# Kernel tuning notes

Measured on AMD Instinct MI355X. Metric: run time of the kernel, lower is better.

Reference implementation:

```python
import jax, jax.numpy as jnp
import numpy as np

B, S, V = 512, 256, 10      # batch, s_node_num, v_node_num
E, H = 128, 128             # embedding, lstm hidden
D = 2 * H                   # num_directions * hidden
PENALTY = 1.0e6
STD = 0.1


def _cell(x, h, c, Wih, Whh, b):
    # PyTorch LSTM cell, gate order i, f, g, o; b = b_ih + b_hh
    g = x @ Wih.T + h @ Whh.T + b
    i, f, gg, o = jnp.split(g, 4, axis=-1)
    c = jax.nn.sigmoid(f) * c + jax.nn.sigmoid(i) * jnp.tanh(gg)
    h = jax.nn.sigmoid(o) * jnp.tanh(c)
    return h, c


def setup_inputs() -> dict:
    key = jax.random.key(0)
    ks = jax.random.split(key, 25)
    w = lambda k, shp: (jax.random.normal(k, shp, jnp.float32) * STD)
    return {
        's_node_indexes': jax.random.randint(ks[0], (B, S), 0, S, dtype=jnp.int32),
        's_inputs': jax.random.uniform(ks[1], (B, S, 3), jnp.float32),
        'v_input': jax.random.uniform(ks[2], (V, 3), jnp.float32) * 0.5,
        'W_embed': w(ks[3], (E, 1)),
        'enc_Wih_f': w(ks[4], (4 * H, E)), 'enc_Whh_f': w(ks[5], (4 * H, H)), 'enc_b_f': w(ks[6], (4 * H,)),
        'enc_Wih_b': w(ks[7], (4 * H, E)), 'enc_Whh_b': w(ks[8], (4 * H, H)), 'enc_b_b': w(ks[9], (4 * H,)),
        'dec_Wih_f': w(ks[10], (4 * H, D)), 'dec_Whh_f': w(ks[11], (4 * H, H)), 'dec_b_f': w(ks[12], (4 * H,)),
        'dec_Wih_b': w(ks[13], (4 * H, D)), 'dec_Whh_b': w(ks[14], (4 * H, H)), 'dec_b_b': w(ks[15], (4 * H,)),
        'W_ref': w(ks[16], (D, D)), 'W_q': w(ks[17], (D, D)), 'v_w': w(ks[18], (D,)),
        'W_ref2': w(ks[19], (D, D)), 'W_q2': w(ks[20], (D, D)), 'v2_w': w(ks[21], (D,)),
    }


def reference(s_node_indexes, s_inputs, v_input, W_embed,
              enc_Wih_f, enc_Whh_f, enc_b_f, enc_Wih_b, enc_Whh_b, enc_b_b,
              dec_Wih_f, dec_Whh_f, dec_b_f, dec_Wih_b, dec_Whh_b, dec_b_b,
              W_ref, W_q, v_w, W_ref2, W_q2, v2_w):
    Bn, Sn = s_node_indexes.shape
    # Embed: snode resource -> Linear(1, E, bias=False)
    emb = s_inputs[:, :, 0:1] @ W_embed.T            # (B, S, E)
    xs = jnp.swapaxes(emb, 0, 1)                     # (S, B, E)
    h0 = jnp.zeros((Bn, H), jnp.float32)
    c0 = jnp.zeros((Bn, H), jnp.float32)

    def enc_scan(Wih, Whh, b, seq):
        def step(carry, x):
            h, c = carry
            h, c = _cell(x, h, c, Wih, Whh, b)
            return (h, c), h
        (hT, cT), hs = jax.lax.scan(step, (h0, c0), seq)
        return hs, hT, cT

    hs_f, hf, cf = enc_scan(enc_Wih_f, enc_Whh_f, enc_b_f, xs)
    hs_b, hb, cb = enc_scan(enc_Wih_b, enc_Whh_b, enc_b_b, xs[::-1])
    Enc = jnp.swapaxes(jnp.concatenate([hs_f, hs_b[::-1]], axis=-1), 0, 1)  # (B, S, D)
    h_state = jnp.stack([hf, hb])                    # (2, B, H)
    c_state = jnp.stack([cf, cb])

    refE = Enc @ W_ref.T                             # (B, S, D) precomputed (dropout p=0)
    ref2E = Enc @ W_ref2.T

    def dec_step(carry, vcpu):
        dec_in, h, c, played = carry                 # dec_in (B, D)
        hf_, cf_ = _cell(dec_in, h[0], c[0], dec_Wih_f, dec_Whh_f, dec_b_f)
        hb_, cb_ = _cell(dec_in, h[1], c[1], dec_Wih_b, dec_Whh_b, dec_b_b)
        dec_out = jnp.concatenate([hf_, hb_], axis=-1)                       # (B, D)
        cannot = (s_inputs[:, :, 0] < vcpu).astype(jnp.float32) + played     # (B, S)
        ow = jnp.tanh(refE + (dec_out @ W_q.T)[:, None, :]) @ v_w - PENALTY * cannot
        att = jax.nn.softmax(jnp.tanh(ref2E + (dec_in @ W_q2.T)[:, None, :]) @ v2_w, axis=1)
        new_in = jnp.einsum('bs,bsd->bd', att, Enc)
        sel = jnp.argmax(ow, axis=1)
        played = played + jax.nn.one_hot(sel, Sn, dtype=jnp.float32)
        return (new_in, jnp.stack([hf_, hb_]), jnp.stack([cf_, cb_]), played), (ow, sel)

    init = (jnp.zeros((Bn, D), jnp.float32), h_state, c_state, jnp.zeros((Bn, Sn), jnp.float32))
    _, (output_weights, sels) = jax.lax.scan(dec_step, init, v_input[:, 0])
    shuffled = sels.T                                # (B, V)
    original = jnp.take_along_axis(s_node_indexes, shuffled, axis=1)
    return original, shuffled, output_weights        # output_weights: (V, B, S)
```

## Files before the change

kernel.cpp:

```cpp
#include <hip/hip_runtime.h>
#include <math.h>

#define cB 512
#define cS 256
#define cV 10
#define cE 128
#define cH 128
#define cD 256
#define cG 512
#define PEN 1.0e6f
#define S1 224
#define PADK 40

typedef _Float16 half8_t __attribute__((ext_vector_type(8)));
typedef _Float16 half4_t __attribute__((ext_vector_type(4)));
typedef float f32x4 __attribute__((ext_vector_type(4)));

#define DOT4(acc, wv, hv)                                   \
    do {                                                    \
        acc = fmaf((wv).x, (hv).x, acc);                    \
        acc = fmaf((wv).y, (hv).y, acc);                    \
        acc = fmaf((wv).z, (hv).z, acc);                    \
        acc = fmaf((wv).w, (hv).w, acc);                    \
    } while (0)

__device__ __forceinline__ float sigmf(float x) { return 1.0f / (1.0f + expf(-x)); }

__global__ __launch_bounds__(512, 1) void k_encoder(
    const float* __restrict__ s_inputs, const float* __restrict__ W_embed,
    const float* __restrict__ Wih_f, const float* __restrict__ Whh_f, const float* __restrict__ b_f,
    const float* __restrict__ Wih_b, const float* __restrict__ Whh_b, const float* __restrict__ b_b,
    _Float16* __restrict__ Ehi, _Float16* __restrict__ Elo,
    float* __restrict__ h_state, float* __restrict__ c_state)
{
    const int dir = blockIdx.x >> 8;
    const int b0  = (blockIdx.x & 255) * 2;
    const float* __restrict__ Wih = dir ? Wih_b : Wih_f;
    const float* __restrict__ Whh = dir ? Whh_b : Whh_f;
    const float* __restrict__ bv  = dir ? b_b   : b_f;
    const int j = threadIdx.x;

    __shared__ __align__(16) float a_in[2][cS];
    __shared__ __align__(16) float hbuf[2][cH];
    __shared__ __align__(16) float gbuf[2][cG];

    {
        int bb = j >> 8, s = j & 255;
        a_in[bb][s] = s_inputs[((size_t)(b0 + bb) * cS + s) * 3];
    }

    float4 w[32];
#pragma unroll
    for (int kk = 0; kk < 32; ++kk) {
        w[kk] = *(const float4*)&Whh[(size_t)j * cH + kk * 4];
        asm volatile("" : "+v"(w[kk].x), "+v"(w[kk].y), "+v"(w[kk].z), "+v"(w[kk].w));
    }

    float u = 0.0f;
#pragma unroll 8
    for (int e = 0; e < cE; ++e) u = fmaf(Wih[(size_t)j * cE + e], W_embed[e], u);
    const float bj = bv[j];

    const int uk = j & 127, ub = (j >> 7) & 1;
    float c_reg = 0.0f;
    float h_last = 0.0f;
    if (j < 256) hbuf[ub][uk] = 0.0f;
    __syncthreads();

    for (int p = 0; p < cS; ++p) {
        const int s = dir ? (cS - 1 - p) : p;
        float acc0 = fmaf(a_in[0][s], u, bj);
        float acc1 = fmaf(a_in[1][s], u, bj);
#pragma unroll
        for (int kk = 0; kk < 32; ++kk) {
            const float4 wv = w[kk];
            const float4 h0 = *(const float4*)&hbuf[0][kk * 4];
            const float4 h1 = *(const float4*)&hbuf[1][kk * 4];
            DOT4(acc0, wv, h0);
            DOT4(acc1, wv, h1);
        }
        gbuf[0][j] = acc0;
        gbuf[1][j] = acc1;
        __syncthreads();

        if (j < 256) {
            float gi = gbuf[ub][uk];
            float gf = gbuf[ub][128 + uk];
            float gg = gbuf[ub][256 + uk];
            float go = gbuf[ub][384 + uk];
            float i_ = sigmf(gi), f_ = sigmf(gf), g_ = tanhf(gg), o_ = sigmf(go);
            c_reg = fmaf(f_, c_reg, i_ * g_);
            float hn = o_ * tanhf(c_reg);
            h_last = hn;
            hbuf[ub][uk] = hn;
            const size_t eidx = ((size_t)(b0 + ub) * cS + s) * cD + dir * cH + uk;
            _Float16 hh = (_Float16)hn;
            Ehi[eidx] = hh;
            Elo[eidx] = (_Float16)(hn - (float)hh);
        }
        __syncthreads();
    }
    if (j < 256) {
        h_state[((size_t)dir * cB + b0 + ub) * cH + uk] = h_last;
        c_state[((size_t)dir * cB + b0 + ub) * cH + uk] = c_reg;
    }
}

__global__ void k_split_w(const float* __restrict__ W1, const float* __restrict__ W2,
                          _Float16* __restrict__ Whi1, _Float16* __restrict__ Wlo1,
                          _Float16* __restrict__ Whi2, _Float16* __restrict__ Wlo2)
{
    const int i = blockIdx.x * 256 + threadIdx.x;
    {
        float a = W1[i]; _Float16 h = (_Float16)a;
        Whi1[i] = h; Wlo1[i] = (_Float16)(a - (float)h);
    }
    {
        float a = W2[i]; _Float16 h = (_Float16)a;
        Whi2[i] = h; Wlo2[i] = (_Float16)(a - (float)h);
    }
}

__global__ __launch_bounds__(256) void k_head_mat(
    const _Float16* __restrict__ Ahi, const _Float16* __restrict__ Alo,
    const _Float16* __restrict__ Whi, const _Float16* __restrict__ Wlo,
    float* __restrict__ outv)
{
    const int tid = threadIdx.x;
    const int w = tid >> 6, l = tid & 63;
    const int m0 = blockIdx.x * 64;

    __shared__ __align__(16) _Float16 As[2][64][PADK];
    __shared__ __align__(16) _Float16 Ws[2][256][PADK];

    const int r = tid >> 2, kq = tid & 3;
    size_t arow;
    {
        const int m = m0 + r;
        const int s = m >> 9, b = m & 511;
        arow = ((size_t)b * cS + s) * cD;
    }
    const size_t wrow = (size_t)tid * cD;

    f32x4 acc[16];
#pragma unroll
    for (int i = 0; i < 16; ++i) acc[i] = (f32x4){0.f, 0.f, 0.f, 0.f};

    const int fr = w * 16 + (l & 15);
    const int kc = (l >> 4) * 8;

    for (int k0 = 0; k0 < 256; k0 += 32) {
        __syncthreads();
        *(uint4*)&As[0][r][kq * 8] = *(const uint4*)&Ahi[arow + k0 + kq * 8];
        *(uint4*)&As[1][r][kq * 8] = *(const uint4*)&Alo[arow + k0 + kq * 8];
#pragma unroll
        for (int q4 = 0; q4 < 4; ++q4) {
            *(uint4*)&Ws[0][tid][q4 * 8] = *(const uint4*)&Whi[wrow + k0 + q4 * 8];
            *(uint4*)&Ws[1][tid][q4 * 8] = *(const uint4*)&Wlo[wrow + k0 + q4 * 8];
        }
        __syncthreads();

        const half8_t ahi = *(const half8_t*)&As[0][fr][kc];
        const half8_t alo = *(const half8_t*)&As[1][fr][kc];
#pragma unroll
        for (int nf = 0; nf < 16; ++nf) {
            const int n = nf * 16 + (l & 15);
            const half8_t bhi = *(const half8_t*)&Ws[0][n][kc];
            const half8_t blo = *(const half8_t*)&Ws[1][n][kc];
            acc[nf] = __builtin_amdgcn_mfma_f32_16x16x32_f16(ahi, bhi, acc[nf], 0, 0, 0);
            acc[nf] = __builtin_amdgcn_mfma_f32_16x16x32_f16(ahi, blo, acc[nf], 0, 0, 0);
            acc[nf] = __builtin_amdgcn_mfma_f32_16x16x32_f16(alo, bhi, acc[nf], 0, 0, 0);
        }
    }
#pragma unroll
    for (int nf = 0; nf < 16; ++nf)
#pragma unroll
        for (int rr = 0; rr < 4; ++rr) {
            const int m = w * 16 + ((l >> 4) << 2) + rr;
            outv[(size_t)(m0 + m) * cD + nf * 16 + (l & 15)] = acc[nf][rr];
        }
}

template <int MODE>
__global__ __launch_bounds__(512, 2) void k_head2(
    const _Float16* __restrict__ Ahi, const _Float16* __restrict__ Alo,
    const _Float16* __restrict__ Whi, const _Float16* __restrict__ Wlo,
    const float* __restrict__ qv, const float* __restrict__ vv,
    float* __restrict__ outv)
{
    const int tid = threadIdx.x;
    const int l = tid & 63;
    const int w = tid >> 6;
    const int wm = w >> 2, wn = w & 3;
    const int g = l >> 4, li = l & 15;
    const int m0 = blockIdx.x * 128;

    __shared__ __align__(16) _Float16 Ah[128][PADK];
    __shared__ __align__(16) _Float16 Al[128][PADK];
    __shared__ __align__(16) _Float16 Wh[256][PADK];
    __shared__ __align__(16) _Float16 Wl[256][PADK];
    __shared__ __align__(16) float qs[4][cD];
    __shared__ __align__(16) float vs[cD];
    __shared__ float spart[4][128];

    if (MODE == 0) {
        const int b = m0 >> 8;
        if (tid < 256) qs[0][tid] = qv[(size_t)b * cD + tid];
        else           vs[tid - 256] = vv[tid - 256];
    } else {
        const int b0 = m0 >> 5;
        qs[tid >> 8][tid & 255] = qv[(size_t)(b0 + (tid >> 8)) * cD + (tid & 255)];
        const int i2 = tid + 512;
        qs[i2 >> 8][i2 & 255] = qv[(size_t)(b0 + (i2 >> 8)) * cD + (i2 & 255)];
        if (tid < 256) vs[tid] = vv[tid];
    }

    const int ar = tid >> 2, aq = tid & 3;
    size_t arow;
    {
        const int m = m0 + ar;
        if (MODE == 0) arow = (size_t)m * cD;
        else { const int b = m >> 5, s = S1 + (m & 31); arow = ((size_t)b * cS + s) * cD; }
    }

    f32x4 acc[4][4];
#pragma unroll
    for (int mi = 0; mi < 4; ++mi)
#pragma unroll
        for (int ni = 0; ni < 4; ++ni) acc[mi][ni] = (f32x4){0.f, 0.f, 0.f, 0.f};

    for (int k0 = 0; k0 < 256; k0 += 32) {
        __syncthreads();
        *(uint4*)&Ah[ar][aq * 8] = *(const uint4*)&Ahi[arow + k0 + aq * 8];
        *(uint4*)&Al[ar][aq * 8] = *(const uint4*)&Alo[arow + k0 + aq * 8];
        *(uint4*)&Wh[ar][aq * 8] = *(const uint4*)&Whi[(size_t)ar * cD + k0 + aq * 8];
        *(uint4*)&Wl[ar][aq * 8] = *(const uint4*)&Wlo[(size_t)ar * cD + k0 + aq * 8];
        *(uint4*)&Wh[ar + 128][aq * 8] = *(const uint4*)&Whi[(size_t)(ar + 128) * cD + k0 + aq * 8];
        *(uint4*)&Wl[ar + 128][aq * 8] = *(const uint4*)&Wlo[(size_t)(ar + 128) * cD + k0 + aq * 8];
        __syncthreads();

        half8_t ah[4], al[4];
#pragma unroll
        for (int mi = 0; mi < 4; ++mi) {
            ah[mi] = *(const half8_t*)&Ah[wm * 64 + mi * 16 + li][g * 8];
            al[mi] = *(const half8_t*)&Al[wm * 64 + mi * 16 + li][g * 8];
        }
#pragma unroll
        for (int ni = 0; ni < 4; ++ni) {
            const half8_t bh = *(const half8_t*)&Wh[wn * 64 + ni * 16 + li][g * 8];
            const half8_t bl = *(const half8_t*)&Wl[wn * 64 + ni * 16 + li][g * 8];
#pragma unroll
            for (int mi = 0; mi < 4; ++mi) {
                acc[mi][ni] = __builtin_amdgcn_mfma_f32_16x16x32_f16(ah[mi], bh, acc[mi][ni], 0, 0, 0);
                acc[mi][ni] = __builtin_amdgcn_mfma_f32_16x16x32_f16(ah[mi], bl, acc[mi][ni], 0, 0, 0);
                acc[mi][ni] = __builtin_amdgcn_mfma_f32_16x16x32_f16(al[mi], bh, acc[mi][ni], 0, 0, 0);
            }
        }
    }

    float val = 0.f;
#pragma unroll
    for (int mi = 0; mi < 4; ++mi)
#pragma unroll
        for (int rr = 0; rr < 4; ++rr) {
            const int row = wm * 64 + mi * 16 + g * 4 + rr;
            const int bl = (MODE == 1) ? (row >> 5) : 0;
            float p = 0.f;
#pragma unroll
            for (int ni = 0; ni < 4; ++ni) {
                const int c = wn * 64 + ni * 16 + li;
                p = fmaf(vs[c], tanhf(acc[mi][ni][rr] + qs[bl][c]), p);
            }
            p += __shfl_xor(p, 1);
            p += __shfl_xor(p, 2);
            p += __shfl_xor(p, 4);
            p += __shfl_xor(p, 8);
            if (li == mi * 4 + rr) val = p;
        }
    {
        const int row_out = wm * 64 + (li >> 2) * 16 + g * 4 + (li & 3);
        spart[wn][row_out] = val;
    }
    __syncthreads();
    if (tid < 128)
        outv[m0 + tid] = spart[0][tid] + spart[1][tid] + spart[2][tid] + spart[3][tid];
}

__global__ __launch_bounds__(256, 4) void k_fold(
    const float* __restrict__ refC, const float* __restrict__ q1v,
    const float* __restrict__ v_w, float* __restrict__ sc1lo)
{
    const int tid = threadIdx.x;
    const int m0 = blockIdx.x * 64;
    const int r = tid >> 2, p = tid & 3;
    const int m = m0 + r;
    const int b = m & 511;
    __shared__ float red[64][4];

    const float* row  = refC + (size_t)m * cD + p * 64;
    const float* qrow = q1v + (size_t)b * cD + p * 64;
    const float* vrow = v_w + p * 64;
    float s = 0.f;
#pragma unroll 4
    for (int d = 0; d < 64; d += 4) {
        const float4 rv4 = *(const float4*)&row[d];
        const float4 q4  = *(const float4*)&qrow[d];
        const float4 v4  = *(const float4*)&vrow[d];
        s = fmaf(v4.x, tanhf(rv4.x + q4.x), s);
        s = fmaf(v4.y, tanhf(rv4.y + q4.y), s);
        s = fmaf(v4.z, tanhf(rv4.z + q4.z), s);
        s = fmaf(v4.w, tanhf(rv4.w + q4.w), s);
    }
    red[r][p] = s;
    __syncthreads();
    if (tid < 64)
        sc1lo[m0 + tid] = red[tid][0] + red[tid][1] + red[tid][2] + red[tid][3];
}

__global__ __launch_bounds__(512, 2) void k_dec_cells(
    const float* __restrict__ dec_in,
    const float* __restrict__ Wih_f, const float* __restrict__ Whh_f, const float* __restrict__ b_f,
    const float* __restrict__ Wih_b, const float* __restrict__ Whh_b, const float* __restrict__ b_b,
    float* __restrict__ h_state, float* __restrict__ c_state, float* __restrict__ dec_out)
{
    const int cell = blockIdx.x >> 7;
    const int b0 = (blockIdx.x & 127) * 4;
    const float* __restrict__ Wih = cell ? Wih_b : Wih_f;
    const float* __restrict__ Whh = cell ? Whh_b : Whh_f;
    const float* __restrict__ bv  = cell ? b_b   : b_f;
    const int j = threadIdx.x;

    __shared__ __align__(16) float xin[4][cD];
    __shared__ __align__(16) float hin[4][cH];
    __shared__ __align__(16) float gbuf[4][cG];

    for (int idx = j; idx < 4 * cD; idx += 512) {
        int bb = idx >> 8, k = idx & 255;
        xin[bb][k] = dec_in[(size_t)(b0 + bb) * cD + k];
    }
    {
        int bb = j >> 7, k = j & 127;
        hin[bb][k] = h_state[((size_t)cell * cB + b0 + bb) * cH + k];
    }
    __syncthreads();

    float a0 = bv[j];
    float a1 = a0, a2 = a0, a3 = a0;
#pragma unroll 4
    for (int kk = 0; kk < 64; ++kk) {
        const float4 wv = *(const float4*)&Wih[(size_t)j * cD + kk * 4];
        const float4 x0 = *(const float4*)&xin[0][kk * 4]; DOT4(a0, wv, x0);
        const float4 x1 = *(const float4*)&xin[1][kk * 4]; DOT4(a1, wv, x1);
        const float4 x2 = *(const float4*)&xin[2][kk * 4]; DOT4(a2, wv, x2);
        const float4 x3 = *(const float4*)&xin[3][kk * 4]; DOT4(a3, wv, x3);
    }
#pragma unroll 4
    for (int kk = 0; kk < 32; ++kk) {
        const float4 wv = *(const float4*)&Whh[(size_t)j * cH + kk * 4];
        const float4 h0 = *(const float4*)&hin[0][kk * 4]; DOT4(a0, wv, h0);
        const float4 h1 = *(const float4*)&hin[1][kk * 4]; DOT4(a1, wv, h1);
        const float4 h2 = *(const float4*)&hin[2][kk * 4]; DOT4(a2, wv, h2);
        const float4 h3 = *(const float4*)&hin[3][kk * 4]; DOT4(a3, wv, h3);
    }
    gbuf[0][j] = a0; gbuf[1][j] = a1; gbuf[2][j] = a2; gbuf[3][j] = a3;
    __syncthreads();

    const int uk = j & 127, ub = j >> 7;
    const float gi = gbuf[ub][uk];
    const float gf = gbuf[ub][128 + uk];
    const float gg = gbuf[ub][256 + uk];
    const float go = gbuf[ub][384 + uk];
    const size_t sidx = ((size_t)cell * cB + b0 + ub) * cH + uk;
    const float c_old = c_state[sidx];
    const float i_ = sigmf(gi), f_ = sigmf(gf), g_ = tanhf(gg), o_ = sigmf(go);
    const float cn = fmaf(f_, c_old, i_ * g_);
    const float hn = o_ * tanhf(cn);
    c_state[sidx] = cn;
    h_state[sidx] = hn;
    dec_out[(size_t)(b0 + ub) * cD + cell * cH + uk] = hn;
}

__global__ __launch_bounds__(256, 2) void k_qproj(
    const float* __restrict__ dec_out, const float* __restrict__ dec_in_old,
    const float* __restrict__ W_q, const float* __restrict__ W_q2,
    float* __restrict__ q1v, float* __restrict__ q2v)
{
    const int b = blockIdx.x;
    const int tid = threadIdx.x;
    __shared__ __align__(16) float dout[cD];
    __shared__ __align__(16) float din[cD];
    dout[tid] = dec_out[(size_t)b * cD + tid];
    din[tid]  = dec_in_old[(size_t)b * cD + tid];
    __syncthreads();
    float s1 = 0.0f, s2 = 0.0f;
#pragma unroll 4
    for (int kk = 0; kk < 64; ++kk) {
        const float4 w1 = *(const float4*)&W_q[(size_t)tid * cD + kk * 4];
        const float4 w2 = *(const float4*)&W_q2[(size_t)tid * cD + kk * 4];
        const float4 x1 = *(const float4*)&dout[kk * 4];
        const float4 x2 = *(const float4*)&din[kk * 4];
        DOT4(s1, w1, x1);
        DOT4(s2, w2, x2);
    }
    q1v[(size_t)b * cD + tid] = s1;
    q2v[(size_t)b * cD + tid] = s2;
}

__global__ __launch_bounds__(256, 2) void k_finish(
    const float* __restrict__ sc1lo, const float* __restrict__ sc1hi,
    const float* __restrict__ sc2,
    const _Float16* __restrict__ Ehi, const _Float16* __restrict__ Elo,
    const float* __restrict__ s_inputs, const int* __restrict__ s_node_indexes,
    const float* __restrict__ v_input, float* __restrict__ played,
    float* __restrict__ dec_in_new, float* __restrict__ outp, int t)
{
    const int b = blockIdx.x;
    const int tid = threadIdx.x;
    const int lane = tid & 63;
    const int wv = tid >> 6;

    __shared__ __align__(16) float atr[cS];
    __shared__ __align__(16) float part[4][cD];
    __shared__ float rv[cS];
    __shared__ int   ri[cS];

    const float owv = (tid < S1) ? sc1lo[(size_t)tid * cB + b]
                                 : sc1hi[(size_t)b * (cS - S1) + (tid - S1)];
    atr[tid] = sc2[(size_t)b * cS + tid];

    const float vcpu = v_input[t * 3];
    float val;
    {
        const float a0 = s_inputs[((size_t)b * cS + tid) * 3];
        const float can = (a0 < vcpu ? 1.0f : 0.0f) + played[(size_t)b * cS + tid];
        val = owv - PEN * can;
        outp[2 * cB * cV + ((size_t)t * cB + b) * cS + tid] = val;
    }
    rv[tid] = val; ri[tid] = tid;
    __syncthreads();
#pragma unroll
    for (int off = 128; off > 0; off >>= 1) {
        if (tid < off) {
            const float v2 = rv[tid + off]; const int i2 = ri[tid + off];
            const float v1 = rv[tid];       const int i1 = ri[tid];
            if (v2 > v1 || (v2 == v1 && i2 < i1)) { rv[tid] = v2; ri[tid] = i2; }
        }
        __syncthreads();
    }
    const int sel = ri[0];
    __syncthreads();
    if (tid == 0) {
        played[(size_t)b * cS + sel] += 1.0f;
        outp[(size_t)b * cV + t] = (float)s_node_indexes[(size_t)b * cS + sel];
        outp[(size_t)cB * cV + (size_t)b * cV + t] = (float)sel;
    }

    rv[tid] = atr[tid];
    __syncthreads();
#pragma unroll
    for (int off = 128; off > 0; off >>= 1) {
        if (tid < off) { const float v2 = rv[tid + off]; if (v2 > rv[tid]) rv[tid] = v2; }
        __syncthreads();
    }
    const float mx = rv[0];
    __syncthreads();
    const float ex = expf(atr[tid] - mx);
    rv[tid] = ex;
    __syncthreads();
#pragma unroll
    for (int off = 128; off > 0; off >>= 1) {
        if (tid < off) rv[tid] += rv[tid + off];
        __syncthreads();
    }
    const float ssum = rv[0];
    __syncthreads();
    atr[tid] = ex / ssum;
    __syncthreads();

    {
        float4 acc = make_float4(0.f, 0.f, 0.f, 0.f);
        for (int s2i = wv * 64; s2i < wv * 64 + 64; ++s2i) {
            const float a = atr[s2i];
            const size_t eidx = ((size_t)b * cS + s2i) * cD + lane * 4;
            const half4_t h4 = *(const half4_t*)&Ehi[eidx];
            const half4_t l4 = *(const half4_t*)&Elo[eidx];
            acc.x = fmaf(a, (float)h4[0] + (float)l4[0], acc.x);
            acc.y = fmaf(a, (float)h4[1] + (float)l4[1], acc.y);
            acc.z = fmaf(a, (float)h4[2] + (float)l4[2], acc.z);
            acc.w = fmaf(a, (float)h4[3] + (float)l4[3], acc.w);
        }
        *(float4*)&part[wv][lane * 4] = acc;
    }
    __syncthreads();
    dec_in_new[(size_t)b * cD + tid] =
        part[0][tid] + part[1][tid] + part[2][tid] + part[3][tid];
}

extern "C" void kernel_launch(void* const* d_in, const int* in_sizes, int n_in,
                              void* d_out, int out_size, void* d_ws, size_t ws_size,
                              hipStream_t stream)
{
    (void)in_sizes; (void)n_in; (void)out_size; (void)ws_size;

    const int*   s_node = (const int*)  d_in[0];
    const float* s_inp  = (const float*)d_in[1];
    const float* v_inp  = (const float*)d_in[2];
    const float* W_emb  = (const float*)d_in[3];
    const float* eWih_f = (const float*)d_in[4];
    const float* eWhh_f = (const float*)d_in[5];
    const float* eb_f   = (const float*)d_in[6];
    const float* eWih_b = (const float*)d_in[7];
    const float* eWhh_b = (const float*)d_in[8];
    const float* eb_b   = (const float*)d_in[9];
    const float* dWih_f = (const float*)d_in[10];
    const float* dWhh_f = (const float*)d_in[11];
    const float* db_f   = (const float*)d_in[12];
    const float* dWih_b = (const float*)d_in[13];
    const float* dWhh_b = (const float*)d_in[14];
    const float* db_b   = (const float*)d_in[15];
    const float* W_ref  = (const float*)d_in[16];
    const float* W_q    = (const float*)d_in[17];
    const float* v_w    = (const float*)d_in[18];
    const float* W_ref2 = (const float*)d_in[19];
    const float* W_q2   = (const float*)d_in[20];
    const float* v2_w   = (const float*)d_in[21];

    float* out = (float*)d_out;
    const size_t ENCSZ = (size_t)cB * cS * cD;
    const size_t SMALL = (size_t)cB * cD;

    char* p = (char*)d_ws;
    _Float16* Ehi = (_Float16*)p; p += ENCSZ * 2;
    _Float16* Elo = (_Float16*)p; p += ENCSZ * 2;
    float* refC  = (float*)p;     p += (size_t)S1 * cB * cD * 4;
    _Float16* Whi1 = (_Float16*)p; p += (size_t)cD * cD * 2;
    _Float16* Wlo1 = (_Float16*)p; p += (size_t)cD * cD * 2;
    _Float16* Whi2 = (_Float16*)p; p += (size_t)cD * cD * 2;
    _Float16* Wlo2 = (_Float16*)p; p += (size_t)cD * cD * 2;
    float* hst    = (float*)p; p += SMALL * 4;
    float* cst    = (float*)p; p += SMALL * 4;
    float* din0   = (float*)p; p += SMALL * 4;
    float* din1   = (float*)p; p += SMALL * 4;
    float* doutb  = (float*)p; p += SMALL * 4;
    float* played = (float*)p; p += SMALL * 4;
    float* q1v    = (float*)p; p += SMALL * 4;
    float* q2v    = (float*)p; p += SMALL * 4;
    float* sc2    = (float*)p; p += SMALL * 4;
    float* sc1lo  = (float*)p; p += (size_t)S1 * cB * 4;
    float* sc1hi  = (float*)p; p += (size_t)(cS - S1) * cB * 4;

    hipMemsetAsync(played, 0, SMALL * sizeof(float), stream);
    hipMemsetAsync(din0,   0, SMALL * sizeof(float), stream);

    k_split_w<<<256, 256, 0, stream>>>(W_ref, W_ref2, Whi1, Wlo1, Whi2, Wlo2);

    k_encoder<<<512, 512, 0, stream>>>(s_inp, W_emb, eWih_f, eWhh_f, eb_f,
                                       eWih_b, eWhh_b, eb_b, Ehi, Elo, hst, cst);

    k_head_mat<<<(S1 * cB) / 64, 256, 0, stream>>>(Ehi, Elo, Whi1, Wlo1, refC);

    for (int t = 0; t < cV; ++t) {
        float* di_old = (t & 1) ? din1 : din0;
        float* di_new = (t & 1) ? din0 : din1;
        k_dec_cells<<<256, 512, 0, stream>>>(di_old, dWih_f, dWhh_f, db_f,
                                             dWih_b, dWhh_b, db_b, hst, cst, doutb);
        k_qproj<<<512, 256, 0, stream>>>(doutb, di_old, W_q, W_q2, q1v, q2v);
        k_head2<0><<<(cB * cS) / 128, 512, 0, stream>>>(Ehi, Elo, Whi2, Wlo2,
                                                        q2v, v2_w, sc2);
        k_head2<1><<<(cB * (cS - S1)) / 128, 512, 0, stream>>>(Ehi, Elo, Whi1, Wlo1,
                                                               q1v, v_w, sc1hi);
        k_fold<<<(S1 * cB) / 64, 256, 0, stream>>>(refC, q1v, v_w, sc1lo);

        k_finish<<<512, 256, 0, stream>>>(sc1lo, sc1hi, sc2, Ehi, Elo,
                                          s_inp, s_node, v_inp, played, di_new, out, t);
    }
}
```

Measured before the change: 3.656 ms.

## Restructure encoder LSTM: 4 batch rows per block, split-K across thread halves

The encoder kernel now processes four batch rows per block with 1024 threads. Each half of the threads handles 64 of the 128 hidden-state columns, and the two partial gate sums are combined through shared memory. The input-projection vector u is precomputed once by a small new kernel instead of being recomputed in every block. The aim is to halve the block count and the weight registers per thread while reusing each weight load across more batch rows. The cost is an extra shared-memory reduction each step and 1024-thread barriers on the sequential 256-step recurrence.

```diff
diff --git a/kernel.cpp b/kernel.cpp
--- a/kernel.cpp
+++ b/kernel.cpp
@@ -26,83 +26,96 @@
 
 __device__ __forceinline__ float sigmf(float x) { return 1.0f / (1.0f + expf(-x)); }
 
-__global__ __launch_bounds__(512, 1) void k_encoder(
-    const float* __restrict__ s_inputs, const float* __restrict__ W_embed,
-    const float* __restrict__ Wih_f, const float* __restrict__ Whh_f, const float* __restrict__ b_f,
-    const float* __restrict__ Wih_b, const float* __restrict__ Whh_b, const float* __restrict__ b_b,
+__global__ void k_uprep(const float* __restrict__ Wih_f, const float* __restrict__ Wih_b,
+                        const float* __restrict__ W_embed, float* __restrict__ uvec)
+{
+    const int j = threadIdx.x;
+    const float* __restrict__ Wih = blockIdx.x ? Wih_b : Wih_f;
+    float u = 0.f;
+#pragma unroll 8
+    for (int e = 0; e < cE; ++e) u = fmaf(Wih[(size_t)j * cE + e], W_embed[e], u);
+    uvec[blockIdx.x * cG + j] = u;
+}
+
+__global__ __launch_bounds__(1024, 4) void k_encoder(
+    const float* __restrict__ s_inputs, const float* __restrict__ uvec,
+    const float* __restrict__ Whh_f, const float* __restrict__ b_f,
+    const float* __restrict__ Whh_b, const float* __restrict__ b_b,
     _Float16* __restrict__ Ehi, _Float16* __restrict__ Elo,
     float* __restrict__ h_state, float* __restrict__ c_state)
 {
-    const int dir = blockIdx.x >> 8;
-    const int b0  = (blockIdx.x & 255) * 2;
-    const float* __restrict__ Wih = dir ? Wih_b : Wih_f;
+    const int dir = blockIdx.x >> 7;
+    const int b0  = (blockIdx.x & 127) * 4;
     const float* __restrict__ Whh = dir ? Whh_b : Whh_f;
     const float* __restrict__ bv  = dir ? b_b   : b_f;
-    const int j = threadIdx.x;
-
-    __shared__ __align__(16) float a_in[2][cS];
-    __shared__ __align__(16) float hbuf[2][cH];
-    __shared__ __align__(16) float gbuf[2][cG];
-
-    {
-        int bb = j >> 8, s = j & 255;
-        a_in[bb][s] = s_inputs[((size_t)(b0 + bb) * cS + s) * 3];
-    }
-
-    float4 w[32];
-#pragma unroll
-    for (int kk = 0; kk < 32; ++kk) {
-        w[kk] = *(const float4*)&Whh[(size_t)j * cH + kk * 4];
-        asm volatile("" : "+v"(w[kk].x), "+v"(w[kk].y), "+v"(w[kk].z), "+v"(w[kk].w));
-    }
-
-    float u = 0.0f;
-#pragma unroll 8
-    for (int e = 0; e < cE; ++e) u = fmaf(Wih[(size_t)j * cE + e], W_embed[e], u);
-    const float bj = bv[j];
-
-    const int uk = j & 127, ub = (j >> 7) & 1;
-    float c_reg = 0.0f;
-    float h_last = 0.0f;
-    if (j < 256) hbuf[ub][uk] = 0.0f;
+    const int tid = threadIdx.x;
+    const int j = tid & 511;
+    const int hf = tid >> 9;
+
+    __shared__ __align__(16) float a_in[4][cS];
+    __shared__ __align__(16) float hbuf[4][cH];
+    __shared__ __align__(16) float gpart[4][2][516];
+
+    a_in[tid >> 8][tid & 255] =
+        s_inputs[((size_t)(b0 + (tid >> 8)) * cS + (tid & 255)) * 3];
+
+    float4 w[16];
+#pragma unroll
+    for (int kk = 0; kk < 16; ++kk)
+        w[kk] = *(const float4*)&Whh[(size_t)j * cH + hf * 64 + kk * 4];
+
+    const float uj = (hf == 0) ? uvec[dir * cG + j] : 0.f;
+    const float bj = (hf == 0) ? bv[j] : 0.f;
+
+    const int ur = tid >> 7, uk = tid & 127;
+    float c_reg = 0.f, h_last = 0.f;
+    if (tid < 512) hbuf[ur][uk] = 0.f;
     __syncthreads();
 
     for (int p = 0; p < cS; ++p) {
         const int s = dir ? (cS - 1 - p) : p;
-        float acc0 = fmaf(a_in[0][s], u, bj);
-        float acc1 = fmaf(a_in[1][s], u, bj);
-#pragma unroll
-        for (int kk = 0; kk < 32; ++kk) {
+        float acc0 = fmaf(a_in[0][s], uj, bj);
+        float acc1 = fmaf(a_in[1][s], uj, bj);
+        float acc2 = fmaf(a_in[2][s], uj, bj);
+        float acc3 = fmaf(a_in[3][s], uj, bj);
+#pragma unroll
+        for (int kk = 0; kk < 16; ++kk) {
             const float4 wv = w[kk];
-            const float4 h0 = *(const float4*)&hbuf[0][kk * 4];
-            const float4 h1 = *(const float4*)&hbuf[1][kk * 4];
+            const float4 h0 = *(const float4*)&hbuf[0][hf * 64 + kk * 4];
             DOT4(acc0, wv, h0);
+            const float4 h1 = *(const float4*)&hbuf[1][hf * 64 + kk * 4];
             DOT4(acc1, wv, h1);
-        }
-        gbuf[0][j] = acc0;
-        gbuf[1][j] = acc1;
-        __syncthreads();
-
-        if (j < 256) {
-            float gi = gbuf[ub][uk];
-            float gf = gbuf[ub][128 + uk];
-            float gg = gbuf[ub][256 + uk];
-            float go = gbuf[ub][384 + uk];
-            float i_ = sigmf(gi), f_ = sigmf(gf), g_ = tanhf(gg), o_ = sigmf(go);
+            const float4 h2 = *(const float4*)&hbuf[2][hf * 64 + kk * 4];
+            DOT4(acc2, wv, h2);
+            const float4 h3 = *(const float4*)&hbuf[3][hf * 64 + kk * 4];
+            DOT4(acc3, wv, h3);
+        }
+        gpart[0][hf][j] = acc0;
+        gpart[1][hf][j] = acc1;
+        gpart[2][hf][j] = acc2;
+        gpart[3][hf][j] = acc3;
+        __syncthreads();
+
+        if (tid < 512) {
+            const float gi = gpart[ur][0][uk]       + gpart[ur][1][uk];
+            const float gf = gpart[ur][0][128 + uk] + gpart[ur][1][128 + uk];
+            const float gg = gpart[ur][0][256 + uk] + gpart[ur][1][256 + uk];
+            const float go = gpart[ur][0][384 + uk] + gpart[ur][1][384 + uk];
+            const float i_ = sigmf(gi), f_ = sigmf(gf), g_ = tanhf(gg), o_ = sigmf(go);
             c_reg = fmaf(f_, c_reg, i_ * g_);
-            float hn = o_ * tanhf(c_reg);
+            const float hn = o_ * tanhf(c_reg);
             h_last = hn;
-            hbuf[ub][uk] = hn;
-            const size_t eidx = ((size_t)(b0 + ub) * cS + s) * cD + dir * cH + uk;
-            _Float16 hh = (_Float16)hn;
+            hbuf[ur][uk] = hn;
+            const size_t eidx = ((size_t)(b0 + ur) * cS + s) * cD + dir * cH + uk;
+            const _Float16 hh = (_Float16)hn;
             Ehi[eidx] = hh;
             Elo[eidx] = (_Float16)(hn - (float)hh);
         }
         __syncthreads();
     }
-    if (j < 256) {
-        h_state[((size_t)dir * cB + b0 + ub) * cH + uk] = h_last;
-        c_state[((size_t)dir * cB + b0 + ub) * cH + uk] = c_reg;
+    if (tid < 512) {
+        h_state[((size_t)dir * cB + b0 + ur) * cH + uk] = h_last;
+        c_state[((size_t)dir * cB + b0 + ur) * cH + uk] = c_reg;
     }
 }
 
@@ -548,14 +561,16 @@
     float* sc2    = (float*)p; p += SMALL * 4;
     float* sc1lo  = (float*)p; p += (size_t)S1 * cB * 4;
     float* sc1hi  = (float*)p; p += (size_t)(cS - S1) * cB * 4;
+    float* uvec   = (float*)p; p += 2 * cG * 4;
 
     hipMemsetAsync(played, 0, SMALL * sizeof(float), stream);
     hipMemsetAsync(din0,   0, SMALL * sizeof(float), stream);
 
     k_split_w<<<256, 256, 0, stream>>>(W_ref, W_ref2, Whi1, Wlo1, Whi2, Wlo2);
-
-    k_encoder<<<512, 512, 0, stream>>>(s_inp, W_emb, eWih_f, eWhh_f, eb_f,
-                                       eWih_b, eWhh_b, eb_b, Ehi, Elo, hst, cst);
+    k_uprep<<<2, 512, 0, stream>>>(eWih_f, eWih_b, W_emb, uvec);
+
+    k_encoder<<<256, 1024, 0, stream>>>(s_inp, uvec, eWhh_f, eb_f, eWhh_b, eb_b,
+                                        Ehi, Elo, hst, cst);
 
     k_head_mat<<<(S1 * cB) / 64, 256, 0, stream>>>(Ehi, Elo, Whi1, Wlo1, refC);
 
```

Result: faster. 3.468 ms (-5.1%).
